# Kernel tuning notes

Hardware: AMD Instinct MI355X
Metric: run time of the kernel (lower is better)

## Reference

```python
import jax, jax.numpy as jnp
import numpy as np

B, T, F, D = 2, 1, 2112, 1024
H, DH = 8, 64
INNER = H * DH
NL = 721           # cls_dim(1) + num_latents(720)
VD = 64            # vis_dim // 4
DEPTH = 6
MAX_FRAMES = 2160
EPS = 1e-5
W_SCALE = 0.02


def _ln(x, g, b):
    m = jnp.mean(x, axis=-1, keepdims=True)
    v = jnp.mean(jnp.square(x - m), axis=-1, keepdims=True)
    return (x - m) * jax.lax.rsqrt(v + EPS) * g + b


def setup_inputs() -> dict:
    key = jax.random.key(0)
    ks = jax.random.split(key, 12)
    n = lambda k, shape, s=1.0: jax.random.normal(k, shape, dtype=jnp.float32) * s
    inp = {}
    inp['x'] = n(ks[0], (B, T, F, D))
    inp['split_sizes'] = jax.random.randint(ks[1], (B,), 0, F, dtype=jnp.int32)
    # resampler parameters (randn init like torch)
    inp['latents'] = n(ks[2], (NL, D))
    inp['spatial_embs'] = n(ks[3], (VD + 1, D))
    inp['frame_embs'] = n(ks[4], (MAX_FRAMES, D))
    # per-layer attention params (stacked over depth)
    inp['nm_g'] = jnp.ones((DEPTH, D)); inp['nm_b'] = jnp.zeros((DEPTH, D))
    inp['nl_g'] = jnp.ones((DEPTH, D)); inp['nl_b'] = jnp.zeros((DEPTH, D))
    inp['wq'] = n(ks[5], (DEPTH, D, INNER), W_SCALE)
    inp['wkv'] = n(ks[6], (DEPTH, D, 2 * INNER), W_SCALE)
    inp['wo'] = n(ks[7], (DEPTH, INNER, D), W_SCALE)
    # per-layer FFN params
    inp['ffn_g'] = jnp.ones((DEPTH, D)); inp['ffn_b'] = jnp.zeros((DEPTH, D))
    inp['ffw1'] = n(ks[8], (DEPTH, D, 4 * D), W_SCALE)
    inp['ffw2'] = n(ks[9], (DEPTH, 4 * D, D), W_SCALE)
    # final norm
    inp['final_g'] = jnp.ones((D,)); inp['final_b'] = jnp.zeros((D,))
    return inp


def reference(x, split_sizes, latents, spatial_embs, frame_embs,
              nm_g, nm_b, nl_g, nl_b, wq, wkv, wo,
              ffn_g, ffn_b, ffw1, ffw2, final_g, final_b):
    b, t, f, d = x.shape
    # spatial embeddings: first VD tokens get rows [:VD], rest get row [VD] broadcast
    add_sp = jnp.concatenate(
        [spatial_embs[:VD], jnp.broadcast_to(spatial_embs[VD:VD + 1], (f - VD, d))], axis=0)
    # frame embeddings: first VD tokens get row 0, frames get rows 1..f-VD
    add_fr = jnp.concatenate(
        [jnp.broadcast_to(frame_embs[0:1], (VD, d)), frame_embs[1:f - VD + 1]], axis=0)
    x = x + (add_sp + add_fr)  # broadcast over (b, t)

    lat = jnp.broadcast_to(latents, (b, t, NL, d))

    # variable-length mask over the x part of KV; latent positions never masked
    mask_x = jnp.arange(f)[None, :] >= split_sizes[:, None]              # (b, f)
    mask = jnp.concatenate([mask_x, jnp.zeros((b, NL), dtype=bool)], -1)  # (b, f+NL)
    mask = mask[:, None, None, None, :]                                   # (b,1,1,1,j)
    scale = DH ** -0.5

    for l in range(DEPTH):
        # --- PerceiverAttention ---
        xn = _ln(x, nm_g[l], nm_b[l])
        latn = _ln(lat, nl_g[l], nl_b[l])
        q = (latn @ wq[l]).reshape(b, t, NL, H, DH) * scale
        kv = jnp.concatenate([xn, latn], axis=-2) @ wkv[l]               # (b,t,f+NL,2*inner)
        k, v = jnp.split(kv, 2, axis=-1)
        k = k.reshape(b, t, f + NL, H, DH)
        v = v.reshape(b, t, f + NL, H, DH)
        sim = jnp.einsum('btihd,btjhd->bhtij', q, k)                     # (b,h,t,NL,f+NL)
        sim = sim - jax.lax.stop_gradient(jnp.max(sim, axis=-1, keepdims=True))
        sim = jnp.where(mask, -jnp.inf, sim)
        attn = jax.nn.softmax(sim, axis=-1)
        o = jnp.einsum('bhtij,btjhd->btihd', attn, v).reshape(b, t, NL, INNER)
        lat = lat + o @ wo[l]
        # --- FeedForward ---
        h1 = _ln(lat, ffn_g[l], ffn_b[l]) @ ffw1[l]
        lat = lat + jax.nn.gelu(h1, approximate=False) @ ffw2[l]

    return _ln(lat, final_g, final_b)
```

## Files before the change

kernel.cpp:

```cpp
#include <hip/hip_runtime.h>
#include <math.h>

constexpr int B = 2;
constexpr int F = 2112;
constexpr int D = 1024;
constexpr int H = 8;
constexpr int DH = 64;
constexpr int INNER = H * DH;
constexpr int NL = 721;
constexpr int NL_PAD = 768;
constexpr int MLAT = B * NL;
constexpr int MLAT_PAD = 1536;
constexpr int VD = 64;
constexpr int DEPTH = 6;
constexpr int FN = F + NL;
constexpr int FN_PAD = 2880;
constexpr int NBH = B * H;
constexpr int SKVMAX = 8;
constexpr int MX = B * F;
constexpr int NBIAS = 6656;
constexpr float EPS = 1e-5f;

typedef __bf16 bf16x8 __attribute__((ext_vector_type(8)));
typedef float  f32x4  __attribute__((ext_vector_type(4)));

static __device__ __forceinline__ unsigned short f2bf(float f)
{
    union { float f; unsigned int u; } x; x.f = f;
    unsigned int r = x.u + 0x7FFFu + ((x.u >> 16) & 1u);
    return (unsigned short)(r >> 16);
}
static __device__ __forceinline__ float bf2f(unsigned short u)
{
    union { unsigned int i; float f; } x; x.i = ((unsigned int)u) << 16; return x.f;
}

static __device__ __forceinline__ int xcd_swz(int b, int nt)
{
    return (b & 7) * (nt >> 3) + (b >> 3);
}

__device__ __forceinline__ void block_reduce_2(float& s, float& ss, float* red)
{
#pragma unroll
    for (int off = 32; off; off >>= 1) {
        s  += __shfl_xor(s, off);
        ss += __shfl_xor(ss, off);
    }
    int wv = threadIdx.x >> 6;
    if ((threadIdx.x & 63) == 0) { red[wv] = s; red[4 + wv] = ss; }
    __syncthreads();
    s  = red[0] + red[1] + red[2] + red[3];
    ss = red[4] + red[5] + red[6] + red[7];
}

__global__ __launch_bounds__(256) void emb_ln_kernel(
    const float* __restrict__ x, const float* __restrict__ sp_emb,
    const float* __restrict__ fr_emb, unsigned short* __restrict__ xhat)
{
    __shared__ float red[8];
    int r = blockIdx.x;
    int j = r % F;
    int t = threadIdx.x;
    const float4* xr = (const float4*)(x + (long)r * D);
    int spr = (j < VD) ? j : VD;
    int frr = (j < VD) ? 0 : (j - VD + 1);
    const float4* sp4 = (const float4*)(sp_emb + (long)spr * D);
    const float4* fr4 = (const float4*)(fr_emb + (long)frr * D);
    float4 v = xr[t], a = sp4[t], c = fr4[t];
    v.x += a.x + c.x; v.y += a.y + c.y; v.z += a.z + c.z; v.w += a.w + c.w;
    float s  = v.x + v.y + v.z + v.w;
    float ss = v.x*v.x + v.y*v.y + v.z*v.z + v.w*v.w;
    block_reduce_2(s, ss, red);
    float mean = s * (1.0f / D);
    float var  = ss * (1.0f / D) - mean * mean;
    float rstd = rsqrtf(var + EPS);
    ushort4 o;
    o.x = f2bf((v.x - mean) * rstd);
    o.y = f2bf((v.y - mean) * rstd);
    o.z = f2bf((v.z - mean) * rstd);
    o.w = f2bf((v.w - mean) * rstd);
    ((ushort4*)(xhat + (long)r * D))[t] = o;
}

__global__ __launch_bounds__(256) void rownorm_plain_kernel(
    const float* __restrict__ in, unsigned short* __restrict__ out)
{
    __shared__ float red[8];
    int r = blockIdx.x;
    int t = threadIdx.x;
    float4 v = ((const float4*)(in + (long)r * D))[t];
    float s  = v.x + v.y + v.z + v.w;
    float ss = v.x*v.x + v.y*v.y + v.z*v.z + v.w*v.w;
    block_reduce_2(s, ss, red);
    float mean = s * (1.0f / D);
    float var  = ss * (1.0f / D) - mean * mean;
    float rstd = rsqrtf(var + EPS);
    ushort4 o;
    o.x = f2bf((v.x - mean) * rstd);
    o.y = f2bf((v.y - mean) * rstd);
    o.z = f2bf((v.z - mean) * rstd);
    o.w = f2bf((v.w - mean) * rstd);
    ((ushort4*)(out + (long)r * D))[t] = o;
}

__global__ __launch_bounds__(256) void final_ln_kernel(
    const float* __restrict__ in, const float* __restrict__ g,
    const float* __restrict__ b, float* __restrict__ out)
{
    __shared__ float red[8];
    int r = blockIdx.x;
    int t = threadIdx.x;
    float4 v = ((const float4*)(in + (long)r * D))[t];
    float s  = v.x + v.y + v.z + v.w;
    float ss = v.x*v.x + v.y*v.y + v.z*v.z + v.w*v.w;
    block_reduce_2(s, ss, red);
    float mean = s * (1.0f / D);
    float var  = ss * (1.0f / D) - mean * mean;
    float rstd = rsqrtf(var + EPS);
    float4 g4 = ((const float4*)g)[t];
    float4 b4 = ((const float4*)b)[t];
    float4 o;
    o.x = (v.x - mean) * rstd * g4.x + b4.x;
    o.y = (v.y - mean) * rstd * g4.y + b4.y;
    o.z = (v.z - mean) * rstd * g4.z + b4.z;
    o.w = (v.w - mean) * rstd * g4.w + b4.w;
    ((float4*)(out + (long)r * D))[t] = o;
}

__global__ __launch_bounds__(256) void lat_init_kernel(
    const float* __restrict__ latents, float* __restrict__ lat)
{
    int r = blockIdx.x;
    int i = r % NL;
    int t = threadIdx.x;
    ((float4*)(lat + (long)r * D))[t] = ((const float4*)(latents + (long)i * D))[t];
}

__global__ __launch_bounds__(256) void bias_kernel(
    const float* __restrict__ wq, const float* __restrict__ wkv,
    const float* __restrict__ ffw1,
    const float* __restrict__ nl_b, const float* __restrict__ nm_b,
    const float* __restrict__ ffn_b, float* __restrict__ bias)
{
    int l = blockIdx.z;
    int o = blockIdx.x * 256 + threadIdx.x;
    int k0 = blockIdx.y * 128;
    const float* W; const float* bv; int n, Nd;
    if (o < 512)       { W = wq   + (long)l * D * INNER;     bv = nl_b  + (long)l * D; n = o;        Nd = INNER; }
    else if (o < 1536) { W = wkv  + (long)l * D * 2 * INNER; bv = nl_b  + (long)l * D; n = o - 512;  Nd = 2 * INNER; }
    else if (o < 2560) { W = wkv  + (long)l * D * 2 * INNER; bv = nm_b  + (long)l * D; n = o - 1536; Nd = 2 * INNER; }
    else               { W = ffw1 + (long)l * D * 4 * D;     bv = ffn_b + (long)l * D; n = o - 2560; Nd = 4 * D; }
    float s = 0.f;
#pragma unroll 4
    for (int k = k0; k < k0 + 128; ++k)
        s += bv[k] * W[(long)k * Nd + n];
    unsafeAtomicAdd(&bias[(long)l * NBIAS + o], s);
}

constexpr long WL_LAT = 1536L * 1024;
constexpr long WL_KVX = 1024L * 1024;
constexpr long WL_WO  = 1024L * 512;
constexpr long WL_F1  = 4096L * 1024;
constexpr long WL_F2  = 1024L * 4096;
constexpr long WL_SZ  = WL_LAT + WL_KVX + WL_WO + WL_F1 + WL_F2;

__device__ __forceinline__ void conv_tile64(
    const float* __restrict__ src, unsigned short* __restrict__ dst,
    int Kd, int Nd, int tn, int tk, const float* __restrict__ g, float* lds)
{
    int t = threadIdx.x;
    int n0 = tn * 64, k0 = tk * 64;
#pragma unroll
    for (int p = 0; p < 16; ++p) {
        int idx = p * 256 + t;
        int kr = idx >> 6, nc = idx & 63;
        float val = src[(long)(k0 + kr) * Nd + n0 + nc];
        if (g) val *= g[k0 + kr];
        lds[nc * 65 + kr] = val;
    }
    __syncthreads();
#pragma unroll
    for (int p = 0; p < 2; ++p) {
        int nl_ = p * 32 + (t >> 3);
        int kc  = t & 7;
        unsigned short u[8];
#pragma unroll
        for (int j = 0; j < 8; ++j)
            u[j] = f2bf(lds[nl_ * 65 + kc * 8 + j]);
        *(uint4*)(dst + (long)(n0 + nl_) * Kd + k0 + kc * 8) = *(uint4*)u;
    }
}

__global__ __launch_bounds__(256) void wt_conv_all_kernel(
    const float* __restrict__ wq, const float* __restrict__ wkv,
    const float* __restrict__ wo, const float* __restrict__ ffw1,
    const float* __restrict__ ffw2,
    const float* __restrict__ nl_g, const float* __restrict__ nm_g,
    const float* __restrict__ ffn_g,
    unsigned short* __restrict__ wbuf, long wstride, int layer0)
{
    __shared__ float lds[64 * 65];
    int l = layer0 + blockIdx.y;
    unsigned short* wl = wbuf + (long)blockIdx.y * wstride;
    const float* wq_l   = wq   + (long)l * D * INNER;
    const float* wkv_l  = wkv  + (long)l * D * 2 * INNER;
    const float* wo_l   = wo   + (long)l * INNER * D;
    const float* ffw1_l = ffw1 + (long)l * D * 4 * D;
    const float* ffw2_l = ffw2 + (long)l * 4 * D * D;
    const float* nlg = nl_g + (long)l * D;
    const float* nmg = nm_g + (long)l * D;
    const float* ffg = ffn_g + (long)l * D;

    int T = blockIdx.x;
    if (T < 128) {
        conv_tile64(wq_l, wl, D, INNER, T & 7, T >> 3, nlg, lds);
    } else if (T < 384) {
        int Ti = T - 128;
        conv_tile64(wkv_l, wl + 512L * D, D, 2 * INNER, Ti & 15, Ti >> 4, nlg, lds);
    } else if (T < 640) {
        int Ti = T - 384;
        conv_tile64(wkv_l, wl + WL_LAT, D, 2 * INNER, Ti & 15, Ti >> 4, nmg, lds);
    } else if (T < 768) {
        int Ti = T - 640;
        conv_tile64(wo_l, wl + WL_LAT + WL_KVX, INNER, D, Ti & 15, Ti >> 4, nullptr, lds);
    } else if (T < 1792) {
        int Ti = T - 768;
        conv_tile64(ffw1_l, wl + WL_LAT + WL_KVX + WL_WO, D, 4 * D, Ti & 63, Ti >> 6, ffg, lds);
    } else {
        int Ti = T - 1792;
        conv_tile64(ffw2_l, wl + WL_LAT + WL_KVX + WL_WO + WL_F1, 4 * D, D, Ti & 15, Ti >> 4, nullptr, lds);
    }
}

__device__ __forceinline__ void load_set(
    const unsigned short* __restrict__ ap, const unsigned short* __restrict__ bp,
    long rs, int ko, bf16x8 (&av)[4], bf16x8 (&bv)[4])
{
#pragma unroll
    for (int q = 0; q < 4; ++q) {
        av[q] = *(const bf16x8*)(ap + q * rs + ko);
        bv[q] = *(const bf16x8*)(bp + q * rs + ko);
    }
}

__device__ __forceinline__ void mfma_set(
    const bf16x8 (&av)[4], const bf16x8 (&bv)[4], f32x4 (&acc)[4][4])
{
#pragma unroll
    for (int mm = 0; mm < 4; ++mm)
#pragma unroll
        for (int nn = 0; nn < 4; ++nn)
            acc[mm][nn] = __builtin_amdgcn_mfma_f32_16x16x32_bf16(av[mm], bv[nn], acc[mm][nn], 0, 0, 0);
}

__device__ __forceinline__ void gemm_core(
    const unsigned short* __restrict__ ap, const unsigned short* __restrict__ bp,
    long rs, int Kc, f32x4 (&acc)[4][4])
{
    bf16x8 aC[4], bC[4], aN[4], bN[4];
    load_set(ap, bp, rs, 0, aC, bC);
    for (int ko = 0; ko < Kc; ko += 64) {
        load_set(ap, bp, rs, ko + 32, aN, bN);
        mfma_set(aC, bC, acc);
        if (ko + 64 < Kc)
            load_set(ap, bp, rs, ko + 64, aC, bC);
        mfma_set(aN, bN, acc);
    }
}

__device__ __forceinline__ bool ksplit_reduce(
    f32x4 (&acc)[4][4], float* red, int w, int lg, int lr)
{
    if (w == 1) {
#pragma unroll
        for (int mm = 0; mm < 4; ++mm)
#pragma unroll
            for (int nn = 0; nn < 4; ++nn)
#pragma unroll
                for (int r = 0; r < 4; ++r)
                    red[(mm * 16 + lg * 4 + r) * 65 + nn * 16 + lr] = acc[mm][nn][r];
    }
    __syncthreads();
    if (w == 0) {
#pragma unroll
        for (int mm = 0; mm < 4; ++mm)
#pragma unroll
            for (int nn = 0; nn < 4; ++nn)
#pragma unroll
                for (int r = 0; r < 4; ++r)
                    acc[mm][nn][r] += red[(mm * 16 + lg * 4 + r) * 65 + nn * 16 + lr];
        return true;
    }
    return false;
}

__global__ __launch_bounds__(128) void qkv_fused_kernel(
    const unsigned short* __restrict__ la, const unsigned short* __restrict__ xhat,
    const unsigned short* __restrict__ wlatT, const float* __restrict__ bias_l,
    unsigned short* __restrict__ qb, unsigned short* __restrict__ kb,
    unsigned short* __restrict__ vt)
{
    __shared__ float red[64 * 65];
    int tid = threadIdx.x;
    int w = tid >> 6, lane = tid & 63;
    int lr = lane & 15, lg = lane >> 4;

    const unsigned short* A;
    const unsigned short* Bt;
    long m0, n0;
    int M, rpb, joff, qcols;
    bool isLat;
    int T = xcd_swz(blockIdx.x, 1608);
    if (T < 552) {
        int bm = T % 23, bn = T / 23;
        A = la; Bt = wlatT;
        m0 = (long)bm * 64; n0 = (long)bn * 64;
        M = MLAT; rpb = NL; joff = F; qcols = 512; isLat = true;
    } else {
        int Ti = T - 552;
        int bm = Ti % 66, bn = Ti / 66;
        A = xhat; Bt = wlatT + WL_LAT;
        m0 = (long)bm * 64; n0 = (long)bn * 64;
        M = MX; rpb = F; joff = 0; qcols = 0; isLat = false;
    }

    const unsigned short* ap = A  + (m0 + lr) * D + w * 512 + lg * 8;
    const unsigned short* bp = Bt + (n0 + lr) * D + w * 512 + lg * 8;
    f32x4 acc[4][4] = {};
    gemm_core(ap, bp, 16L * D, 512, acc);

    if (!ksplit_reduce(acc, red, w, lg, lr)) return;

#pragma unroll
    for (int mm = 0; mm < 4; ++mm) {
        long ar0 = m0 + mm * 16 + lg * 4;
        if (ar0 >= M) continue;
#pragma unroll
        for (int nn = 0; nn < 4; ++nn) {
            long col = n0 + nn * 16 + lr;
            float bcol = isLat ? bias_l[col] : bias_l[1536 + col];
            f32x4 v = acc[mm][nn];
#pragma unroll
            for (int r = 0; r < 4; ++r) v[r] += bcol;
            if (col < qcols) {
#pragma unroll
                for (int r = 0; r < 4; ++r) {
                    long ar = ar0 + r;
                    if (ar < M) {
                        int bb = ar >= NL;
                        long i = ar - (bb ? NL : 0);
                        qb[((long)bb * NL_PAD + i) * INNER + col] = f2bf(v[r] * 0.125f);
                    }
                }
            } else {
                int c = (int)col - qcols;
                if (c < 512) {
#pragma unroll
                    for (int r = 0; r < 4; ++r) {
                        long ar = ar0 + r;
                        if (ar < M) {
                            int bb = ar >= rpb;
                            long i = ar - (bb ? rpb : 0);
                            kb[((long)bb * FN_PAD + joff + i) * INNER + c] = f2bf(v[r]);
                        }
                    }
                } else {
                    int d = c - 512;
                    int bb0 = ar0 >= rpb;
                    int bb3 = (ar0 + 3) >= rpb;
                    long i0 = ar0 - (bb0 ? rpb : 0);
                    long j0 = joff + i0;
                    if ((ar0 + 3 < M) && (bb0 == bb3) && ((j0 & 3) == 0)) {
                        ushort4 pk;
                        pk.x = f2bf(v[0]); pk.y = f2bf(v[1]);
                        pk.z = f2bf(v[2]); pk.w = f2bf(v[3]);
                        *(ushort4*)(vt + ((long)bb0 * INNER + d) * FN_PAD + j0) = pk;
                    } else {
#pragma unroll
                        for (int r = 0; r < 4; ++r) {
                            long ar = ar0 + r;
                            if (ar < M) {
                                int bb = ar >= rpb;
                                long i = ar - (bb ? rpb : 0);
                                vt[((long)bb * INNER + d) * FN_PAD + joff + i] = f2bf(v[r]);
                            }
                        }
                    }
                }
            }
        }
    }
}

__global__ __launch_bounds__(128) void gemm_gelu2_kernel(
    const unsigned short* __restrict__ A, const unsigned short* __restrict__ Bt,
    unsigned short* __restrict__ C, const float* __restrict__ bias,
    int M, int K, int ldc, int bmN)
{
    __shared__ float red[64 * 65];
    int tid = threadIdx.x;
    int w = tid >> 6, lane = tid & 63;
    int lr = lane & 15, lg = lane >> 4;
    int u = xcd_swz(blockIdx.x, gridDim.x);
    int bm = u % bmN, bn = u / bmN;
    long m0 = (long)bm * 64, n0 = (long)bn * 64;
    int kh = K >> 1;

    const unsigned short* ap = A  + (m0 + lr) * K + w * kh + lg * 8;
    const unsigned short* bp = Bt + (n0 + lr) * K + w * kh + lg * 8;
    f32x4 acc[4][4] = {};
    gemm_core(ap, bp, 16L * K, kh, acc);

    if (!ksplit_reduce(acc, red, w, lg, lr)) return;

#pragma unroll
    for (int mm = 0; mm < 4; ++mm) {
        long ar0 = m0 + mm * 16 + lg * 4;
        if (ar0 >= M) continue;
#pragma unroll
        for (int nn = 0; nn < 4; ++nn) {
            long col = n0 + nn * 16 + lr;
            float bcol = bias[col];
            f32x4 v = acc[mm][nn];
#pragma unroll
            for (int r = 0; r < 4; ++r)
                if (ar0 + r < M) {
                    float val = v[r] + bcol;
                    val = 0.5f * val * (1.0f + erff(val * 0.70710678118654752f));
                    C[(ar0 + r) * (long)ldc + col] = f2bf(val);
                }
        }
    }
}

__global__ __launch_bounds__(64) void gemm_split_kernel(
    const unsigned short* __restrict__ A, const unsigned short* __restrict__ Bt,
    float* __restrict__ C, int M, int K, int Kc, int ldc, int bmN, int bnN)
{
    int lane = threadIdx.x;
    int lr = lane & 15, lg = lane >> 4;
    int u = xcd_swz(blockIdx.x, gridDim.x);
    int bm = u % bmN;
    int t2 = u / bmN;
    int bn = t2 % bnN;
    int kz = t2 / bnN;
    long m0 = (long)bm * 64;
    long n0 = (long)bn * 64;
    int k0 = kz * Kc;

    const unsigned short* ap = A  + (m0 + lr) * K + k0 + lg * 8;
    const unsigned short* bp = Bt + (n0 + lr) * K + k0 + lg * 8;
    f32x4 acc[4][4] = {};
    gemm_core(ap, bp, 16L * K, Kc, acc);

#pragma unroll
    for (int mm = 0; mm < 4; ++mm) {
        long ar0 = m0 + mm * 16 + lg * 4;
        if (ar0 >= M) continue;
#pragma unroll
        for (int nn = 0; nn < 4; ++nn) {
            long col = n0 + nn * 16 + lr;
            f32x4 v = acc[mm][nn];
#pragma unroll
            for (int r = 0; r < 4; ++r)
                if (ar0 + r < M)
                    unsafeAtomicAdd(&C[(ar0 + r) * (long)ldc + col], v[r]);
        }
    }
}

__global__ __launch_bounds__(256) void attn_split_kernel(
    const unsigned short* __restrict__ qb, const unsigned short* __restrict__ kb,
    const unsigned short* __restrict__ vt, const int* __restrict__ split,
    float* __restrict__ po, float* __restrict__ pml, int skv)
{
    int u = xcd_swz(blockIdx.x, gridDim.x);
    int q64  = u % 12;
    int bh   = (u / 12) % NBH;
    int sidx = u / (12 * NBH);
    int b  = bh >> 3;
    int h  = bh & 7;
    int w  = threadIdx.x >> 6;
    int lane = threadIdx.x & 63;
    int q0 = q64 * 64 + w * 16;
    if (q0 >= NL) return;

    __shared__ unsigned short p_lds[4][16 * 64];
    unsigned short* pl = p_lds[w];

    int lr = lane & 15;
    int lg = lane >> 4;

    bf16x8 qa0, qa1;
    {
        const unsigned short* qrow = qb + ((long)b * NL_PAD + q0 + lr) * INNER + h * 64;
        qa0 = *(const bf16x8*)(qrow + lg * 8);
        qa1 = *(const bf16x8*)(qrow + 32 + lg * 8);
    }

    f32x4 oacc[4] = {{0,0,0,0},{0,0,0,0},{0,0,0,0},{0,0,0,0}};
    float m[4]    = {-1e30f, -1e30f, -1e30f, -1e30f};
    float lsum[4] = {0.f, 0.f, 0.f, 0.f};

    int sp = split[b];
    if (sp < 0) sp = 0;
    if (sp > F) sp = F;
    int ntx = (sp + 63) >> 6;
    int ntot = ntx + 12;
    int t0 = (ntot * sidx) / skv;
    int t1 = (ntot * (sidx + 1)) / skv;

    for (int t = t0; t < t1; ++t) {
        int j0, limit;
        if (t < ntx) { j0 = t * 64;             limit = sp; }
        else         { j0 = F + (t - ntx) * 64; limit = FN; }

        f32x4 s[4] = {{0,0,0,0},{0,0,0,0},{0,0,0,0},{0,0,0,0}};
        const unsigned short* kbase =
            kb + ((long)b * FN_PAD + j0 + lr) * INNER + h * 64 + lg * 8;
#pragma unroll
        for (int st = 0; st < 4; ++st) {
            bf16x8 kf0 = *(const bf16x8*)(kbase + (long)st * 16 * INNER);
            bf16x8 kf1 = *(const bf16x8*)(kbase + (long)st * 16 * INNER + 32);
            s[st] = __builtin_amdgcn_mfma_f32_16x16x32_bf16(qa0, kf0, s[st], 0, 0, 0);
            s[st] = __builtin_amdgcn_mfma_f32_16x16x32_bf16(qa1, kf1, s[st], 0, 0, 0);
        }

        if (j0 + 64 > limit) {
#pragma unroll
            for (int st = 0; st < 4; ++st) {
                bool valid = (j0 + st * 16 + lr) < limit;
#pragma unroll
                for (int r = 0; r < 4; ++r)
                    s[st][r] = valid ? s[st][r] : -1e30f;
            }
        }

        float tm[4];
#pragma unroll
        for (int r = 0; r < 4; ++r)
            tm[r] = fmaxf(fmaxf(s[0][r], s[1][r]), fmaxf(s[2][r], s[3][r]));
#pragma unroll
        for (int off = 1; off < 16; off <<= 1) {
#pragma unroll
            for (int r = 0; r < 4; ++r)
                tm[r] = fmaxf(tm[r], __shfl_xor(tm[r], off));
        }
        float cr[4];
#pragma unroll
        for (int r = 0; r < 4; ++r) {
            float mn = fmaxf(m[r], tm[r]);
            cr[r] = __expf(m[r] - mn);
            m[r]  = mn;
        }
#pragma unroll
        for (int st = 0; st < 4; ++st)
#pragma unroll
            for (int r = 0; r < 4; ++r)
                s[st][r] = __expf(s[st][r] - m[r]);
        float ts[4];
#pragma unroll
        for (int r = 0; r < 4; ++r)
            ts[r] = (s[0][r] + s[1][r]) + (s[2][r] + s[3][r]);
#pragma unroll
        for (int off = 1; off < 16; off <<= 1) {
#pragma unroll
            for (int r = 0; r < 4; ++r)
                ts[r] += __shfl_xor(ts[r], off);
        }
#pragma unroll
        for (int r = 0; r < 4; ++r)
            lsum[r] = lsum[r] * cr[r] + ts[r];
#pragma unroll
        for (int nst = 0; nst < 4; ++nst)
#pragma unroll
            for (int r = 0; r < 4; ++r)
                oacc[nst][r] *= cr[r];

#pragma unroll
        for (int st = 0; st < 4; ++st)
#pragma unroll
            for (int r = 0; r < 4; ++r) {
                int row  = lg * 4 + r;
                int col  = st * 16 + lr;
                int byte = (row * 128 + col * 2) ^ ((row & 7) << 4);
                *(unsigned short*)((char*)pl + byte) = f2bf(s[st][r]);
            }

#pragma unroll
        for (int kk = 0; kk < 2; ++kk) {
            int row  = lr;
            int byte = (row * 128 + kk * 64 + lg * 16) ^ ((row & 7) << 4);
            bf16x8 pa = *(const bf16x8*)((char*)pl + byte);
#pragma unroll
            for (int nst = 0; nst < 4; ++nst) {
                const unsigned short* vp =
                    vt + ((long)bh * DH + nst * 16 + lr) * FN_PAD + j0 + kk * 32 + lg * 8;
                bf16x8 vf = *(const bf16x8*)vp;
                oacc[nst] = __builtin_amdgcn_mfma_f32_16x16x32_bf16(pa, vf, oacc[nst], 0, 0, 0);
            }
        }
    }

    long base = ((long)sidx * NBH + bh) * NL_PAD;
#pragma unroll
    for (int nst = 0; nst < 4; ++nst)
#pragma unroll
        for (int r = 0; r < 4; ++r) {
            int row = q0 + lg * 4 + r;
            if (row < NL)
                po[(base + row) * DH + nst * 16 + lr] = oacc[nst][r];
        }
    if (lr == 0) {
#pragma unroll
        for (int r = 0; r < 4; ++r) {
            int row = q0 + lg * 4 + r;
            if (row < NL) {
                pml[(base + row) * 2 + 0] = m[r];
                pml[(base + row) * 2 + 1] = lsum[r];
            }
        }
    }
}

__global__ __launch_bounds__(256) void attn_combine_kernel(
    const float* __restrict__ po, const float* __restrict__ pml,
    unsigned short* __restrict__ o, int skv)
{
    int row = blockIdx.x * 4 + (threadIdx.x >> 6);
    if (row >= NBH * NL) return;
    int lane = threadIdx.x & 63;
    int bh = row / NL;
    int i  = row - bh * NL;
    int b = bh >> 3, h = bh & 7;

    float m = -1e30f, l = 0.0f, acc = 0.0f;
    for (int s = 0; s < skv; ++s) {
        long base = ((long)s * NBH + bh) * NL_PAD + i;
        float ms = pml[base * 2 + 0];
        float ls = pml[base * 2 + 1];
        float os = po[base * DH + lane];
        float mn = fmaxf(m, ms);
        float c1 = __expf(m - mn);
        float c2 = __expf(ms - mn);
        acc = acc * c1 + os * c2;
        l   = l * c1 + ls * c2;
        m   = mn;
    }
    o[((long)b * NL + i) * INNER + h * 64 + lane] = f2bf(acc / l);
}

extern "C" void kernel_launch(void* const* d_in, const int* in_sizes, int n_in,
                              void* d_out, int out_size, void* d_ws, size_t ws_size,
                              hipStream_t stream)
{
    const float* x        = (const float*)d_in[0];
    const int*   split    = (const int*)d_in[1];
    const float* latents  = (const float*)d_in[2];
    const float* sp_emb   = (const float*)d_in[3];
    const float* fr_emb   = (const float*)d_in[4];
    const float* nm_g     = (const float*)d_in[5];
    const float* nm_b     = (const float*)d_in[6];
    const float* nl_g     = (const float*)d_in[7];
    const float* nl_b     = (const float*)d_in[8];
    const float* wq       = (const float*)d_in[9];
    const float* wkv      = (const float*)d_in[10];
    const float* wo       = (const float*)d_in[11];
    const float* ffn_g    = (const float*)d_in[12];
    const float* ffn_b    = (const float*)d_in[13];
    const float* ffw1     = (const float*)d_in[14];
    const float* ffw2     = (const float*)d_in[15];
    const float* final_g  = (const float*)d_in[16];
    const float* final_b  = (const float*)d_in[17];
    float* out = (float*)d_out;

    char* cur = (char*)d_ws;
    auto alloc = [&](size_t bytes) {
        void* p = (void*)cur;
        cur += (bytes + 255) & ~(size_t)255;
        return p;
    };

    unsigned short* xhat = (unsigned short*)alloc((long)MX * D * 2);
    float* lat  = (float*)alloc((long)B * NL * D * 4);
    unsigned short* la  = (unsigned short*)alloc((long)MLAT_PAD * D * 2);
    unsigned short* fa  = (unsigned short*)alloc((long)MLAT_PAD * D * 2);
    unsigned short* h1b = (unsigned short*)alloc((long)MLAT_PAD * 4 * D * 2);
    unsigned short* ob  = (unsigned short*)alloc((long)MLAT_PAD * INNER * 2);
    unsigned short* qb  = (unsigned short*)alloc((long)B * NL_PAD * INNER * 2);
    unsigned short* kb  = (unsigned short*)alloc((long)B * FN_PAD * INNER * 2);
    unsigned short* vt  = (unsigned short*)alloc((long)B * FN_PAD * INNER * 2);
    float* bias = (float*)alloc((long)DEPTH * NBIAS * 4);
    float* pml  = (float*)alloc((long)SKVMAX * NBH * NL_PAD * 2 * 4);

    size_t fixed = (size_t)(cur - (char*)d_ws);
    const size_t po8 = ((size_t)8 * NBH * NL_PAD * DH * 4 + 255) & ~(size_t)255;
    const size_t po4 = ((size_t)4 * NBH * NL_PAD * DH * 4 + 255) & ~(size_t)255;
    const size_t wb6 = ((size_t)6 * WL_SZ * 2 + 255) & ~(size_t)255;
    const size_t wb1 = ((size_t)WL_SZ * 2 + 255) & ~(size_t)255;
    const size_t margin = 4096;

    int skv;
    bool hoist_w;
    if (fixed + po8 + wb6 + margin <= ws_size)      { skv = 8; hoist_w = true;  }
    else if (fixed + po4 + wb6 + margin <= ws_size) { skv = 4; hoist_w = true;  }
    else if (fixed + po8 + wb1 + margin <= ws_size) { skv = 8; hoist_w = false; }
    else                                            { skv = 4; hoist_w = false; }

    float* po = (float*)alloc(skv == 8 ? po8 : po4);
    unsigned short* wbuf = (unsigned short*)alloc(hoist_w ? wb6 : wb1);

    hipMemsetAsync(bias, 0, (size_t)DEPTH * NBIAS * 4, stream);

    emb_ln_kernel<<<MX, 256, 0, stream>>>(x, sp_emb, fr_emb, xhat);
    lat_init_kernel<<<B * NL, 256, 0, stream>>>(latents, lat);
    bias_kernel<<<dim3(NBIAS / 256, 8, 6), 256, 0, stream>>>(
        wq, wkv, ffw1, nl_b, nm_b, ffn_b, bias);

    if (hoist_w)
        wt_conv_all_kernel<<<dim3(2816, 6), 256, 0, stream>>>(
            wq, wkv, wo, ffw1, ffw2, nl_g, nm_g, ffn_g, wbuf, WL_SZ, 0);

    for (int l = 0; l < DEPTH; ++l) {
        unsigned short* wl = wbuf + (hoist_w ? (long)l * WL_SZ : 0);
        if (!hoist_w)
            wt_conv_all_kernel<<<dim3(2816, 1), 256, 0, stream>>>(
                wq, wkv, wo, ffw1, ffw2, nl_g, nm_g, ffn_g, wbuf, 0, l);

        unsigned short* wlatT = wl;
        unsigned short* woT   = wl + WL_LAT + WL_KVX;
        unsigned short* f1T   = wl + WL_LAT + WL_KVX + WL_WO;
        unsigned short* f2T   = wl + WL_LAT + WL_KVX + WL_WO + WL_F1;
        const float* bias_l = bias + (long)l * NBIAS;

        rownorm_plain_kernel<<<MLAT, 256, 0, stream>>>(lat, la);

        qkv_fused_kernel<<<1608, 128, 0, stream>>>(la, xhat, wlatT, bias_l, qb, kb, vt);

        attn_split_kernel<<<12 * NBH * skv, 256, 0, stream>>>(
            qb, kb, vt, split, po, pml, skv);
        attn_combine_kernel<<<(NBH * NL + 3) / 4, 256, 0, stream>>>(po, pml, ob, skv);

        gemm_split_kernel<<<23 * 16 * 4, 64, 0, stream>>>(
            ob, woT, lat, MLAT, INNER, 128, D, 23, 16);

        rownorm_plain_kernel<<<MLAT, 256, 0, stream>>>(lat, fa);
        gemm_gelu2_kernel<<<23 * 64, 128, 0, stream>>>(
            fa, f1T, h1b, bias_l + 2560, MLAT, D, 4 * D, 23);
        gemm_split_kernel<<<23 * 16 * 8, 64, 0, stream>>>(
            h1b, f2T, lat, MLAT, 4 * D, 512, D, 23, 16);
    }

    final_ln_kernel<<<MLAT, 256, 0, stream>>>(lat, final_g, final_b, out);
}
```

Baseline: 1.907 ms.

## Overlap next layer's x-side KV GEMM with current FFN2 split GEMM

Separates the x-token K/V projection from the latent QKV kernel and schedules the next layer's x-side KV tiles in the same launch as the current layer's FFW2 split-K GEMM. The x-side KV depends only on the fixed normalized input and the next layer's weights, so it can run alongside the FFN tail to fill the machine. The aim is to shorten the critical path by removing the large x-side work from the QKV stage. In exchange the KV tiles now run with a single wave of 64 threads and no K-split, and the schedule only applies when all layer weights are hoisted.

```diff
diff --git a/kernel.cpp b/kernel.cpp
--- a/kernel.cpp
+++ b/kernel.cpp
@@ -19,6 +19,8 @@
 constexpr int SKVMAX = 8;
 constexpr int MX = B * F;
 constexpr int NBIAS = 6656;
+constexpr int NT_FFW2 = 23 * 16 * 8;
+constexpr int NT_KVX  = 66 * 16;
 constexpr float EPS = 1e-5f;
 
 typedef __bf16 bf16x8 __attribute__((ext_vector_type(8)));
@@ -295,8 +297,73 @@
     return false;
 }
 
-__global__ __launch_bounds__(128) void qkv_fused_kernel(
-    const unsigned short* __restrict__ la, const unsigned short* __restrict__ xhat,
+__device__ __forceinline__ void kvx_tile(
+    int Ti, const unsigned short* __restrict__ xhat,
+    const unsigned short* __restrict__ wkvxT, const float* __restrict__ bias_x,
+    unsigned short* __restrict__ kb, unsigned short* __restrict__ vt, int lane)
+{
+    int lr = lane & 15, lg = lane >> 4;
+    int bm = Ti % 66, bn = Ti / 66;
+    long m0 = (long)bm * 64, n0 = (long)bn * 64;
+
+    const unsigned short* ap = xhat + (m0 + lr) * D + lg * 8;
+    const unsigned short* bp = wkvxT + (n0 + lr) * D + lg * 8;
+    f32x4 acc[4][4] = {};
+    gemm_core(ap, bp, 16L * D, D, acc);
+
+#pragma unroll
+    for (int mm = 0; mm < 4; ++mm) {
+        long ar0 = m0 + mm * 16 + lg * 4;
+        if (ar0 >= MX) continue;
+#pragma unroll
+        for (int nn = 0; nn < 4; ++nn) {
+            long col = n0 + nn * 16 + lr;
+            float bcol = bias_x[col];
+            f32x4 v = acc[mm][nn];
+#pragma unroll
+            for (int r = 0; r < 4; ++r) v[r] += bcol;
+            if (col < 512) {
+#pragma unroll
+                for (int r = 0; r < 4; ++r) {
+                    long ar = ar0 + r;
+                    int bb = ar >= F;
+                    long i = ar - (bb ? F : 0);
+                    kb[((long)bb * FN_PAD + i) * INNER + col] = f2bf(v[r]);
+                }
+            } else {
+                int d = (int)col - 512;
+                int bb0 = ar0 >= F;
+                int bb3 = (ar0 + 3) >= F;
+                long i0 = ar0 - (bb0 ? F : 0);
+                if ((bb0 == bb3) && ((i0 & 3) == 0)) {
+                    ushort4 pk;
+                    pk.x = f2bf(v[0]); pk.y = f2bf(v[1]);
+                    pk.z = f2bf(v[2]); pk.w = f2bf(v[3]);
+                    *(ushort4*)(vt + ((long)bb0 * INNER + d) * FN_PAD + i0) = pk;
+                } else {
+#pragma unroll
+                    for (int r = 0; r < 4; ++r) {
+                        long ar = ar0 + r;
+                        int bb = ar >= F;
+                        long i = ar - (bb ? F : 0);
+                        vt[((long)bb * INNER + d) * FN_PAD + i] = f2bf(v[r]);
+                    }
+                }
+            }
+        }
+    }
+}
+
+__global__ __launch_bounds__(64) void kvx_kernel(
+    const unsigned short* __restrict__ xhat, const unsigned short* __restrict__ wkvxT,
+    const float* __restrict__ bias_x,
+    unsigned short* __restrict__ kb, unsigned short* __restrict__ vt)
+{
+    kvx_tile(xcd_swz(blockIdx.x, NT_KVX), xhat, wkvxT, bias_x, kb, vt, threadIdx.x);
+}
+
+__global__ __launch_bounds__(128) void qlat_kernel(
+    const unsigned short* __restrict__ la,
     const unsigned short* __restrict__ wlatT, const float* __restrict__ bias_l,
     unsigned short* __restrict__ qb, unsigned short* __restrict__ kb,
     unsigned short* __restrict__ vt)
@@ -306,27 +373,12 @@
     int w = tid >> 6, lane = tid & 63;
     int lr = lane & 15, lg = lane >> 4;
 
-    const unsigned short* A;
-    const unsigned short* Bt;
-    long m0, n0;
-    int M, rpb, joff, qcols;
-    bool isLat;
-    int T = xcd_swz(blockIdx.x, 1608);
-    if (T < 552) {
-        int bm = T % 23, bn = T / 23;
-        A = la; Bt = wlatT;
-        m0 = (long)bm * 64; n0 = (long)bn * 64;
-        M = MLAT; rpb = NL; joff = F; qcols = 512; isLat = true;
-    } else {
-        int Ti = T - 552;
-        int bm = Ti % 66, bn = Ti / 66;
-        A = xhat; Bt = wlatT + WL_LAT;
-        m0 = (long)bm * 64; n0 = (long)bn * 64;
-        M = MX; rpb = F; joff = 0; qcols = 0; isLat = false;
-    }
-
-    const unsigned short* ap = A  + (m0 + lr) * D + w * 512 + lg * 8;
-    const unsigned short* bp = Bt + (n0 + lr) * D + w * 512 + lg * 8;
+    int T = xcd_swz(blockIdx.x, 552);
+    int bm = T % 23, bn = T / 23;
+    long m0 = (long)bm * 64, n0 = (long)bn * 64;
+
+    const unsigned short* ap = la    + (m0 + lr) * D + w * 512 + lg * 8;
+    const unsigned short* bp = wlatT + (n0 + lr) * D + w * 512 + lg * 8;
     f32x4 acc[4][4] = {};
     gemm_core(ap, bp, 16L * D, 512, acc);
 
@@ -335,43 +387,43 @@
 #pragma unroll
     for (int mm = 0; mm < 4; ++mm) {
         long ar0 = m0 + mm * 16 + lg * 4;
-        if (ar0 >= M) continue;
+        if (ar0 >= MLAT) continue;
 #pragma unroll
         for (int nn = 0; nn < 4; ++nn) {
             long col = n0 + nn * 16 + lr;
-            float bcol = isLat ? bias_l[col] : bias_l[1536 + col];
+            float bcol = bias_l[col];
             f32x4 v = acc[mm][nn];
 #pragma unroll
             for (int r = 0; r < 4; ++r) v[r] += bcol;
-            if (col < qcols) {
+            if (col < 512) {
 #pragma unroll
                 for (int r = 0; r < 4; ++r) {
                     long ar = ar0 + r;
-                    if (ar < M) {
+                    if (ar < MLAT) {
                         int bb = ar >= NL;
                         long i = ar - (bb ? NL : 0);
                         qb[((long)bb * NL_PAD + i) * INNER + col] = f2bf(v[r] * 0.125f);
                     }
                 }
             } else {
-                int c = (int)col - qcols;
+                int c = (int)col - 512;
                 if (c < 512) {
 #pragma unroll
                     for (int r = 0; r < 4; ++r) {
                         long ar = ar0 + r;
-                        if (ar < M) {
-                            int bb = ar >= rpb;
-                            long i = ar - (bb ? rpb : 0);
-                            kb[((long)bb * FN_PAD + joff + i) * INNER + c] = f2bf(v[r]);
+                        if (ar < MLAT) {
+                            int bb = ar >= NL;
+                            long i = ar - (bb ? NL : 0);
+                            kb[((long)bb * FN_PAD + F + i) * INNER + c] = f2bf(v[r]);
                         }
                     }
                 } else {
                     int d = c - 512;
-                    int bb0 = ar0 >= rpb;
-                    int bb3 = (ar0 + 3) >= rpb;
-                    long i0 = ar0 - (bb0 ? rpb : 0);
-                    long j0 = joff + i0;
-                    if ((ar0 + 3 < M) && (bb0 == bb3) && ((j0 & 3) == 0)) {
+                    int bb0 = ar0 >= NL;
+                    int bb3 = (ar0 + 3) >= NL;
+                    long i0 = ar0 - (bb0 ? NL : 0);
+                    long j0 = F + i0;
+                    if ((ar0 + 3 < MLAT) && (bb0 == bb3) && ((j0 & 3) == 0)) {
                         ushort4 pk;
                         pk.x = f2bf(v[0]); pk.y = f2bf(v[1]);
                         pk.z = f2bf(v[2]); pk.w = f2bf(v[3]);
@@ -380,10 +432,10 @@
 #pragma unroll
                         for (int r = 0; r < 4; ++r) {
                             long ar = ar0 + r;
-                            if (ar < M) {
-                                int bb = ar >= rpb;
-                                long i = ar - (bb ? rpb : 0);
-                                vt[((long)bb * INNER + d) * FN_PAD + joff + i] = f2bf(v[r]);
+                            if (ar < MLAT) {
+                                int bb = ar >= NL;
+                                long i = ar - (bb ? NL : 0);
+                                vt[((long)bb * INNER + d) * FN_PAD + F + i] = f2bf(v[r]);
                             }
                         }
                     }
@@ -434,13 +486,11 @@
     }
 }
 
-__global__ __launch_bounds__(64) void gemm_split_kernel(
-    const unsigned short* __restrict__ A, const unsigned short* __restrict__ Bt,
-    float* __restrict__ C, int M, int K, int Kc, int ldc, int bmN, int bnN)
-{
-    int lane = threadIdx.x;
+__device__ __forceinline__ void resa_tile(
+    int u, const unsigned short* __restrict__ A, const unsigned short* __restrict__ Bt,
+    float* __restrict__ C, int M, int K, int Kc, int ldc, int bmN, int bnN, int lane)
+{
     int lr = lane & 15, lg = lane >> 4;
-    int u = xcd_swz(blockIdx.x, gridDim.x);
     int bm = u % bmN;
     int t2 = u / bmN;
     int bn = t2 % bnN;
@@ -468,6 +518,27 @@
                     unsafeAtomicAdd(&C[(ar0 + r) * (long)ldc + col], v[r]);
         }
     }
+}
+
+__global__ __launch_bounds__(64) void gemm_split_kernel(
+    const unsigned short* __restrict__ A, const unsigned short* __restrict__ Bt,
+    float* __restrict__ C, int M, int K, int Kc, int ldc, int bmN, int bnN)
+{
+    resa_tile(xcd_swz(blockIdx.x, gridDim.x), A, Bt, C, M, K, Kc, ldc, bmN, bnN, threadIdx.x);
+}
+
+__global__ __launch_bounds__(64) void ffw2_kvx_kernel(
+    const unsigned short* __restrict__ h1b, const unsigned short* __restrict__ f2T,
+    float* __restrict__ lat,
+    const unsigned short* __restrict__ xhat, const unsigned short* __restrict__ wkvxT_n,
+    const float* __restrict__ bias_xn,
+    unsigned short* __restrict__ kb, unsigned short* __restrict__ vt)
+{
+    int T = xcd_swz(blockIdx.x, gridDim.x);
+    if (T < NT_FFW2)
+        resa_tile(T, h1b, f2T, lat, MLAT, 4 * D, 512, D, 23, 16, threadIdx.x);
+    else
+        kvx_tile(T - NT_FFW2, xhat, wkvxT_n, bias_xn, kb, vt, threadIdx.x);
 }
 
 __global__ __launch_bounds__(256) void attn_split_kernel(
@@ -722,11 +793,17 @@
         wt_conv_all_kernel<<<dim3(2816, 6), 256, 0, stream>>>(
             wq, wkv, wo, ffw1, ffw2, nl_g, nm_g, ffn_g, wbuf, WL_SZ, 0);
 
+    if (hoist_w)
+        kvx_kernel<<<NT_KVX, 64, 0, stream>>>(xhat, wbuf + WL_LAT, bias + 1536, kb, vt);
+
     for (int l = 0; l < DEPTH; ++l) {
         unsigned short* wl = wbuf + (hoist_w ? (long)l * WL_SZ : 0);
-        if (!hoist_w)
+        if (!hoist_w) {
             wt_conv_all_kernel<<<dim3(2816, 1), 256, 0, stream>>>(
                 wq, wkv, wo, ffw1, ffw2, nl_g, nm_g, ffn_g, wbuf, 0, l);
+            kvx_kernel<<<NT_KVX, 64, 0, stream>>>(
+                xhat, wl + WL_LAT, bias + (long)l * NBIAS + 1536, kb, vt);
+        }
 
         unsigned short* wlatT = wl;
         unsigned short* woT   = wl + WL_LAT + WL_KVX;
@@ -736,7 +813,7 @@
 
         rownorm_plain_kernel<<<MLAT, 256, 0, stream>>>(lat, la);
 
-        qkv_fused_kernel<<<1608, 128, 0, stream>>>(la, xhat, wlatT, bias_l, qb, kb, vt);
+        qlat_kernel<<<552, 128, 0, stream>>>(la, wlatT, bias_l, qb, kb, vt);
 
         attn_split_kernel<<<12 * NBH * skv, 256, 0, stream>>>(
             qb, kb, vt, split, po, pml, skv);
@@ -748,8 +825,16 @@
         rownorm_plain_kernel<<<MLAT, 256, 0, stream>>>(lat, fa);
         gemm_gelu2_kernel<<<23 * 64, 128, 0, stream>>>(
             fa, f1T, h1b, bias_l + 2560, MLAT, D, 4 * D, 23);
-        gemm_split_kernel<<<23 * 16 * 8, 64, 0, stream>>>(
-            h1b, f2T, lat, MLAT, 4 * D, 512, D, 23, 16);
+
+        if (hoist_w && l + 1 < DEPTH) {
+            unsigned short* wkvx_n = wbuf + (long)(l + 1) * WL_SZ + WL_LAT;
+            const float* bias_xn = bias + (long)(l + 1) * NBIAS + 1536;
+            ffw2_kvx_kernel<<<NT_FFW2 + NT_KVX, 64, 0, stream>>>(
+                h1b, f2T, lat, xhat, wkvx_n, bias_xn, kb, vt);
+        } else {
+            gemm_split_kernel<<<NT_FFW2, 64, 0, stream>>>(
+                h1b, f2T, lat, MLAT, 4 * D, 512, D, 23, 16);
+        }
     }
 
     final_ln_kernel<<<MLAT, 256, 0, stream>>>(lat, final_g, final_b, out);
```

New measurement: 2.058 ms, median of 2. 1.08x slower.
